# Performance work log

Hardware: AMD Instinct MI355X
Metric: run time of the kernel (lower is better)

Reference implementation:

```python
import jax, jax.numpy as jnp
import numpy as np

HEADS = 4
DIM_HEAD = 64
EPS = 1e-12  # F.normalize clamp_min eps

def _l2norm(t):
    n = jnp.sqrt(jnp.sum(t * t, axis=-1, keepdims=True))
    return t / jnp.maximum(n, EPS)

def _dwconv3d(x, w, groups):
    # x: [b, c, d, h, w]; w: [c, 1, 3, 3, 3]
    return jax.lax.conv_general_dilated(
        x, w, window_strides=(1, 1, 1),
        padding=((1, 1), (1, 1), (1, 1)),
        dimension_numbers=('NCDHW', 'OIDHW', 'NCDHW'),
        feature_group_count=groups)

def setup_inputs() -> dict:
    key = jax.random.key(0)
    ks = jax.random.split(key, 6)
    dim, inner = 64, HEADS * DIM_HEAD
    x_in = jax.random.normal(ks[0], (1, 8, 128, 128, dim), jnp.float32)
    w_qkv = jax.random.normal(ks[1], (dim, 3 * inner), jnp.float32) * 0.05
    rescale = jnp.ones((HEADS, 1, 1), jnp.float32)
    w_proj = jax.random.normal(ks[2], (inner, dim), jnp.float32) * 0.05
    b_proj = jax.random.normal(ks[3], (dim,), jnp.float32) * 0.01
    w_pe1 = jax.random.normal(ks[4], (dim, 1, 3, 3, 3), jnp.float32) * 0.1
    w_pe2 = jax.random.normal(ks[5], (dim, 1, 3, 3, 3), jnp.float32) * 0.1
    return {"x_in": x_in, "w_qkv": w_qkv, "rescale": rescale,
            "w_proj": w_proj, "b_proj": b_proj, "w_pe1": w_pe1, "w_pe2": w_pe2}

def reference(x_in, w_qkv, rescale, w_proj, b_proj, w_pe1, w_pe2):
    b, d, h, w, c = x_in.shape
    N = d * h * w
    inner = HEADS * DIM_HEAD
    x = x_in.reshape(b, N, c)
    qkv = x @ w_qkv  # [b, N, 3*inner]
    q, k, v = jnp.split(qkv, 3, axis=-1)
    # [b, N, inner] -> [b, heads, dim_head, N]
    to_hdn = lambda t: t.reshape(b, N, HEADS, DIM_HEAD).transpose(0, 2, 3, 1)
    q, k, v = to_hdn(q), to_hdn(k), to_hdn(v)
    q = _l2norm(q)
    k = _l2norm(k)
    attn = jnp.einsum('bhdn,bhen->bhde', k, q)  # [b, heads, dd, dd]
    attn = attn * rescale[None]
    attn = jax.nn.softmax(attn, axis=-1)
    xo = jnp.einsum('bhde,bhen->bhdn', attn, v)  # [b, heads, dd, N]
    xo = xo.transpose(0, 3, 1, 2).reshape(b, N, inner)  # (h dd) channel order
    out_c = (xo @ w_proj + b_proj).reshape(b, d, h, w, c)
    # positional branch: depthwise conv3d -> GELU -> depthwise conv3d
    xp = x_in.transpose(0, 4, 1, 2, 3)  # [b, c, d, h, w]
    xp = _dwconv3d(xp, w_pe1, c)
    xp = jax.nn.gelu(xp, approximate=False)
    xp = _dwconv3d(xp, w_pe2, c)
    out_p = xp.transpose(0, 2, 3, 4, 1)
    return out_c + out_p
```

## Files before the change

### kernel.cpp

```cpp
#include <hip/hip_runtime.h>
#include <hip/hip_bf16.h>
#include <math.h>


#define NTOK 131072

__device__ __forceinline__ uint32_t pk2(float a, float b) {
    return ((__float_as_uint(a) + 0x8000u) >> 16) |
           (((__float_as_uint(b) + 0x8000u) >> 16) << 16);
}
__device__ __forceinline__ float bl(uint32_t w) { return __uint_as_float(w << 16); }
__device__ __forceinline__ float bh(uint32_t w) { return __uint_as_float(w & 0xFFFF0000u); }

__global__ __launch_bounds__(256) void k_gram(const float* __restrict__ x,
                                              float* __restrict__ partial) {
    __shared__ float xs[16][64];
    const int tid = threadIdx.x;
    const int col = tid & 63;
    const int g = tid >> 6;
    float acc[16];
#pragma unroll
    for (int i = 0; i < 16; ++i) acc[i] = 0.f;
    const long tok0 = (long)blockIdx.x * 128;
    for (int t0 = 0; t0 < 128; t0 += 16) {
        __syncthreads();
        const float4* src = (const float4*)(x + (tok0 + t0) * 64);
        ((float4*)&xs[0][0])[tid] = src[tid];
        __syncthreads();
#pragma unroll
        for (int t = 0; t < 16; ++t) {
            const float xa = xs[t][col];
#pragma unroll
            for (int j = 0; j < 16; j += 4) {
                const float4 lv = *(const float4*)&xs[t][g * 16 + j];
                acc[j + 0] += lv.x * xa;
                acc[j + 1] += lv.y * xa;
                acc[j + 2] += lv.z * xa;
                acc[j + 3] += lv.w * xa;
            }
        }
    }
    float* p = partial + (size_t)blockIdx.x * 4096;
#pragma unroll
    for (int i = 0; i < 16; ++i) p[(g * 16 + i) * 64 + col] = acc[i];
}

__global__ __launch_bounds__(256) void k_reduceG(const float* __restrict__ partial,
                                                 float* __restrict__ G) {
    const int pslice = blockIdx.x >> 4;
    const int eblk = blockIdx.x & 15;
    const int e = eblk * 256 + threadIdx.x;
    const float* p = partial + (size_t)pslice * 64 * 4096 + e;
    float s = 0.f;
#pragma unroll 8
    for (int i = 0; i < 64; ++i) s += p[(size_t)i * 4096];
    atomicAdd(&G[e], s);
}

__global__ __launch_bounds__(512) void k_attn(const float* __restrict__ G,
                                              const float* __restrict__ w_qkv,
                                              const float* __restrict__ rescale,
                                              const float* __restrict__ w_proj,
                                              float* __restrict__ wf) {
    __shared__ float smem[6 * 4096 + 64 * 65];
    float (*Gs)[64] = (float(*)[64])smem;
    float (*PT)[64] = (float(*)[64])smem;
    float (*Bq)[64] = (float(*)[64])(smem + 4096);
    float (*Bk)[64] = (float(*)[64])(smem + 8192);
    float (*Bp)[64] = (float(*)[64])(smem + 12288);
    float (*M1)[64] = (float(*)[64])(smem + 16384);
    float (*M2)[64] = (float(*)[64])(smem + 20480);
    float (*Sb)[65] = (float(*)[65])(smem + 24576);
    __shared__ float qin[64], kin[64];

    const int h = blockIdx.x;
    const int tid = threadIdx.x;
    const int lane = tid & 63;
    const int g = tid >> 6;
    const int p0 = g * 8;

    for (int idx = tid; idx < 4096; idx += 512) {
        const int a = idx >> 6, e = idx & 63;
        Gs[a][e] = G[idx];
        Bq[a][e] = w_qkv[a * 768 + h * 64 + e];
        Bk[a][e] = w_qkv[a * 768 + 256 + h * 64 + e];
        Bp[a][e] = w_proj[(h * 64 + a) * 64 + e];
    }
    __syncthreads();

    {
        float acc[8];
#pragma unroll
        for (int i = 0; i < 8; ++i) acc[i] = 0.f;
        for (int a = 0; a < 64; ++a) {
            const float r = Bq[a][lane];
            const float4 l0 = *(const float4*)&Gs[a][p0];
            const float4 l1 = *(const float4*)&Gs[a][p0 + 4];
            acc[0] += l0.x * r; acc[1] += l0.y * r; acc[2] += l0.z * r; acc[3] += l0.w * r;
            acc[4] += l1.x * r; acc[5] += l1.y * r; acc[6] += l1.z * r; acc[7] += l1.w * r;
        }
#pragma unroll
        for (int i = 0; i < 8; ++i) M1[p0 + i][lane] = acc[i];
    }
    {
        float acc[8];
#pragma unroll
        for (int i = 0; i < 8; ++i) acc[i] = 0.f;
        for (int a = 0; a < 64; ++a) {
            const float r = Bk[a][lane];
            const float4 l0 = *(const float4*)&Gs[a][p0];
            const float4 l1 = *(const float4*)&Gs[a][p0 + 4];
            acc[0] += l0.x * r; acc[1] += l0.y * r; acc[2] += l0.z * r; acc[3] += l0.w * r;
            acc[4] += l1.x * r; acc[5] += l1.y * r; acc[6] += l1.z * r; acc[7] += l1.w * r;
        }
#pragma unroll
        for (int i = 0; i < 8; ++i) M2[p0 + i][lane] = acc[i];
    }
    __syncthreads();

    if (tid < 64) {
        float s = 0.f;
        for (int a = 0; a < 64; ++a) s += Bq[a][tid] * M1[a][tid];
        qin[tid] = 1.f / fmaxf(sqrtf(s), 1e-12f);
    } else if (tid < 128) {
        const int d = tid - 64;
        float s = 0.f;
        for (int a = 0; a < 64; ++a) s += Bk[a][d] * M2[a][d];
        kin[d] = 1.f / fmaxf(sqrtf(s), 1e-12f);
    }
    __syncthreads();

    const float rs = rescale[h];
    {
        float acc[8];
#pragma unroll
        for (int i = 0; i < 8; ++i) acc[i] = 0.f;
        for (int a = 0; a < 64; ++a) {
            const float r = M1[a][lane];
            const float4 l0 = *(const float4*)&Bk[a][p0];
            const float4 l1 = *(const float4*)&Bk[a][p0 + 4];
            acc[0] += l0.x * r; acc[1] += l0.y * r; acc[2] += l0.z * r; acc[3] += l0.w * r;
            acc[4] += l1.x * r; acc[5] += l1.y * r; acc[6] += l1.z * r; acc[7] += l1.w * r;
        }
        const float qv = qin[lane] * rs;
#pragma unroll
        for (int i = 0; i < 8; ++i) Sb[p0 + i][lane] = acc[i] * (kin[p0 + i] * qv);
    }
    for (int idx = tid; idx < 4096; idx += 512) {
        const int a = idx >> 6, e = idx & 63;
        Bq[e][a] = w_qkv[a * 768 + 512 + h * 64 + e];
    }
    __syncthreads();

    if (tid < 64) {
        const int d = tid;
        float m = -1e30f;
        for (int e = 0; e < 64; ++e) m = fmaxf(m, Sb[d][e]);
        float s = 0.f;
        for (int e = 0; e < 64; ++e) {
            const float pv = expf(Sb[d][e] - m);
            s += pv;
            PT[e][d] = pv;
        }
        const float inv = 1.f / s;
        for (int e = 0; e < 64; ++e) PT[e][d] *= inv;
    }
    __syncthreads();

    {
        float acc[8];
#pragma unroll
        for (int i = 0; i < 8; ++i) acc[i] = 0.f;
        for (int e = 0; e < 64; ++e) {
            const float r = Bq[e][lane];
            const float4 l0 = *(const float4*)&PT[e][p0];
            const float4 l1 = *(const float4*)&PT[e][p0 + 4];
            acc[0] += l0.x * r; acc[1] += l0.y * r; acc[2] += l0.z * r; acc[3] += l0.w * r;
            acc[4] += l1.x * r; acc[5] += l1.y * r; acc[6] += l1.z * r; acc[7] += l1.w * r;
        }
        __syncthreads();
#pragma unroll
        for (int i = 0; i < 8; ++i) M2[p0 + i][lane] = acc[i];
    }
    __syncthreads();

    {
        float acc[8];
#pragma unroll
        for (int i = 0; i < 8; ++i) acc[i] = 0.f;
        for (int d = 0; d < 64; ++d) {
            const float r = Bp[d][lane];
            const float4 l0 = *(const float4*)&M2[d][p0];
            const float4 l1 = *(const float4*)&M2[d][p0 + 4];
            acc[0] += l0.x * r; acc[1] += l0.y * r; acc[2] += l0.z * r; acc[3] += l0.w * r;
            acc[4] += l1.x * r; acc[5] += l1.y * r; acc[6] += l1.z * r; acc[7] += l1.w * r;
        }
#pragma unroll
        for (int i = 0; i < 8; ++i) atomicAdd(&wf[(p0 + i) * 64 + lane], acc[i]);
    }
}

__global__ __launch_bounds__(256) void k_out(const float* __restrict__ x,
                                             const float* __restrict__ wf_g,
                                             const float* __restrict__ b_proj,
                                             float* __restrict__ out) {
    __shared__ float wfs[64][64];
    __shared__ float xs[64][64];
    const int tid = threadIdx.x;
    const int c = tid & 63;
    const int q = tid >> 6;
    for (int idx = tid; idx < 4096; idx += 256) wfs[idx >> 6][idx & 63] = wf_g[idx];
    __syncthreads();
    float wf[64];
#pragma unroll
    for (int j = 0; j < 64; ++j) wf[j] = wfs[j][c];
    const float bb = b_proj[c];
    const long base = (long)blockIdx.x * 256;
    for (int s = 0; s < 4; ++s) {
        const long v0 = base + s * 64;
        __syncthreads();
        const float4* src = (const float4*)(x + v0 * 64);
#pragma unroll
        for (int r = 0; r < 4; ++r) ((float4*)&xs[0][0])[tid + r * 256] = src[tid + r * 256];
        __syncthreads();
#pragma unroll
        for (int vi = 0; vi < 16; ++vi) {
            const int v = q * 16 + vi;
            float acc = bb;
#pragma unroll
            for (int j = 0; j < 64; j += 4) {
                const float4 xr = *(const float4*)&xs[v][j];
                acc += xr.x * wf[j] + xr.y * wf[j + 1] + xr.z * wf[j + 2] + xr.w * wf[j + 3];
            }
            out[(v0 + v) * 64 + c] = acc;
        }
    }
}

__global__ __launch_bounds__(256) void k_conv(const float* __restrict__ x,
                                              const float* __restrict__ w1,
                                              const float* __restrict__ w2,
                                              float* __restrict__ out) {
    __shared__ uint32_t xt[12][12][8][6];
    __shared__ uint32_t y1[10][10][8][6];
    const int tid = threadIdx.x;
    const int b = blockIdx.x;
    const int xcd = b & 7, seq = (b >> 3) & 31, cg = b >> 8;
    const int tile = xcd * 32 + seq;
    const int tw = tile & 15, th = tile >> 4;
    const int h0 = th * 8, w0 = tw * 8;
    const int c = tid & 7;
    const int cglob = cg * 8 + c;

    float wr1[27];
#pragma unroll
    for (int o = 0; o < 27; ++o) wr1[o] = w1[cglob * 27 + o];

    for (int e = tid; e < 1152; e += 256) {
        const int sp = e >> 3;
        const int hh = sp / 12;
        const int ww = sp - hh * 12;
        const int gh = h0 + hh - 2, gw = w0 + ww - 2;
        uint32_t col[6] = {0u, 0u, 0u, 0u, 0u, 0u};
        if ((unsigned)gh < 128u && (unsigned)gw < 128u) {
            const float* xp = x + ((long)gh * 128 + gw) * 64 + cglob;
            float v[8];
#pragma unroll
            for (int gd = 0; gd < 8; ++gd) v[gd] = xp[(long)gd * 1048576];
            col[1] = pk2(v[0], v[1]);
            col[2] = pk2(v[2], v[3]);
            col[3] = pk2(v[4], v[5]);
            col[4] = pk2(v[6], v[7]);
        }
        uint32_t* dst = &xt[hh][ww][e & 7][0];
        *(uint2*)(dst + 0) = make_uint2(col[0], col[1]);
        *(uint2*)(dst + 2) = make_uint2(col[2], col[3]);
        *(uint2*)(dst + 4) = make_uint2(col[4], col[5]);
    }
    __syncthreads();

    for (int e = tid; e < 800; e += 256) {
        const int sp = e >> 3;
        const int hi_ = sp / 10;
        const int wi = sp - hi_ * 10;
        const int ghp = h0 + hi_ - 1, gwp = w0 + wi - 1;
        uint32_t ow_[6];
        if ((unsigned)ghp < 128u && (unsigned)gwp < 128u) {
            float acc[8];
#pragma unroll
            for (int j = 0; j < 8; ++j) acc[j] = 0.f;
#pragma unroll
            for (int oh = 0; oh < 3; ++oh) {
#pragma unroll
                for (int ow = 0; ow < 3; ++ow) {
                    const uint32_t* cp = &xt[hi_ + oh][wi + ow][e & 7][0];
                    const uint2 wa = *(const uint2*)(cp + 0);
                    const uint2 wb = *(const uint2*)(cp + 2);
                    const uint2 wc = *(const uint2*)(cp + 4);
                    float xc[12];
                    xc[1] = bh(wa.x);
                    xc[2] = bl(wa.y); xc[3] = bh(wa.y);
                    xc[4] = bl(wb.x); xc[5] = bh(wb.x);
                    xc[6] = bl(wb.y); xc[7] = bh(wb.y);
                    xc[8] = bl(wc.x); xc[9] = bh(wc.x);
                    xc[10] = bl(wc.y);
                    const float wg0 = wr1[oh * 3 + ow];
                    const float wg1 = wr1[9 + oh * 3 + ow];
                    const float wg2 = wr1[18 + oh * 3 + ow];
#pragma unroll
                    for (int j = 0; j < 8; ++j)
                        acc[j] += wg0 * xc[j + 1] + wg1 * xc[j + 2] + wg2 * xc[j + 3];
                }
            }
            float gl[8];
#pragma unroll
            for (int j = 0; j < 8; ++j)
                gl[j] = 0.5f * acc[j] * (1.f + erff(acc[j] * 0.70710678118654752f));
            ow_[0] = pk2(0.f, gl[0]);
            ow_[1] = pk2(gl[1], gl[2]);
            ow_[2] = pk2(gl[3], gl[4]);
            ow_[3] = pk2(gl[5], gl[6]);
            ow_[4] = pk2(gl[7], 0.f);
            ow_[5] = 0u;
        } else {
#pragma unroll
            for (int i = 0; i < 6; ++i) ow_[i] = 0u;
        }
        uint32_t* dst = &y1[hi_][wi][e & 7][0];
        *(uint2*)(dst + 0) = make_uint2(ow_[0], ow_[1]);
        *(uint2*)(dst + 2) = make_uint2(ow_[2], ow_[3]);
        *(uint2*)(dst + 4) = make_uint2(ow_[4], ow_[5]);
    }

    float wr2[27];
#pragma unroll
    for (int o = 0; o < 27; ++o) wr2[o] = w2[cglob * 27 + o];
    __syncthreads();

    for (int e = tid; e < 512; e += 256) {
        const int sp = e >> 3;
        const int ho = sp >> 3, wo = sp & 7;
        float a2[8];
#pragma unroll
        for (int j = 0; j < 8; ++j) a2[j] = 0.f;
#pragma unroll
        for (int oh = 0; oh < 3; ++oh) {
#pragma unroll
            for (int ow = 0; ow < 3; ++ow) {
                const uint32_t* cp = &y1[ho + oh][wo + ow][e & 7][0];
                const uint2 wa = *(const uint2*)(cp + 0);
                const uint2 wb = *(const uint2*)(cp + 2);
                const uint32_t wcw = cp[4];
                float yc[10];
                yc[0] = bl(wa.x); yc[1] = bh(wa.x);
                yc[2] = bl(wa.y); yc[3] = bh(wa.y);
                yc[4] = bl(wb.x); yc[5] = bh(wb.x);
                yc[6] = bl(wb.y); yc[7] = bh(wb.y);
                yc[8] = bl(wcw);  yc[9] = bh(wcw);
                const float wg0 = wr2[oh * 3 + ow];
                const float wg1 = wr2[9 + oh * 3 + ow];
                const float wg2 = wr2[18 + oh * 3 + ow];
#pragma unroll
                for (int j = 0; j < 8; ++j)
                    a2[j] += wg0 * yc[j] + wg1 * yc[j + 1] + wg2 * yc[j + 2];
            }
        }
        const int gh = h0 + ho, gw = w0 + wo;
        float* op = out + ((long)gh * 128 + gw) * 64 + cglob;
#pragma unroll
        for (int j = 0; j < 8; ++j) op[(long)j * 1048576] += a2[j];
    }
}

extern "C" void kernel_launch(void* const* d_in, const int* in_sizes, int n_in,
                              void* d_out, int out_size, void* d_ws, size_t ws_size,
                              hipStream_t stream) {
    const float* x       = (const float*)d_in[0];
    const float* w_qkv   = (const float*)d_in[1];
    const float* rescale = (const float*)d_in[2];
    const float* w_proj  = (const float*)d_in[3];
    const float* b_proj  = (const float*)d_in[4];
    const float* w_pe1   = (const float*)d_in[5];
    const float* w_pe2   = (const float*)d_in[6];
    float* out = (float*)d_out;

    float* G  = (float*)d_ws;
    float* wf = G + 4096;
    float* partial = out;

    hipMemsetAsync(G, 0, 8192 * sizeof(float), stream);
    k_gram<<<1024, 256, 0, stream>>>(x, partial);
    k_reduceG<<<256, 256, 0, stream>>>(partial, G);
    k_attn<<<4, 512, 0, stream>>>(G, w_qkv, rescale, w_proj, wf);
    k_out<<<512, 256, 0, stream>>>(x, wf, b_proj, out);
    k_conv<<<2048, 256, 0, stream>>>(x, w_pe1, w_pe2, out);
}
```

Measured before the change: 234.8 us.

## Compute Gram matrix with split-bf16 MFMA and shrink conv LDS layout

The Gram-matrix kernel now uses bf16 MFMA instructions with a hi/lo split of fp32 inputs (three products) to keep near-fp32 accuracy. Only the upper-triangular 16x16 tiles are computed, and the reduce kernel maps symmetric entries back onto them. This replaces the scalar FMA loop with matrix-core work and shrinks the partial buffer. Separately, the conv kernel's LDS column stride drops from 6 to 5 words, which cuts shared-memory footprint and may change bank conflicts, though loads go from uint2 to scalar.

```diff
diff --git a/kernel.cpp b/kernel.cpp
--- a/kernel.cpp
+++ b/kernel.cpp
@@ -5,6 +5,9 @@
 
 #define NTOK 131072
 
+typedef __attribute__((ext_vector_type(8))) short short8v;
+typedef __attribute__((ext_vector_type(4))) float f32x4;
+
 __device__ __forceinline__ uint32_t pk2(float a, float b) {
     return ((__float_as_uint(a) + 0x8000u) >> 16) |
            (((__float_as_uint(b) + 0x8000u) >> 16) << 16);
@@ -14,47 +17,69 @@
 
 __global__ __launch_bounds__(256) void k_gram(const float* __restrict__ x,
                                               float* __restrict__ partial) {
-    __shared__ float xs[16][64];
     const int tid = threadIdx.x;
-    const int col = tid & 63;
-    const int g = tid >> 6;
-    float acc[16];
-#pragma unroll
-    for (int i = 0; i < 16; ++i) acc[i] = 0.f;
-    const long tok0 = (long)blockIdx.x * 128;
-    for (int t0 = 0; t0 < 128; t0 += 16) {
-        __syncthreads();
-        const float4* src = (const float4*)(x + (tok0 + t0) * 64);
-        ((float4*)&xs[0][0])[tid] = src[tid];
-        __syncthreads();
-#pragma unroll
-        for (int t = 0; t < 16; ++t) {
-            const float xa = xs[t][col];
-#pragma unroll
-            for (int j = 0; j < 16; j += 4) {
-                const float4 lv = *(const float4*)&xs[t][g * 16 + j];
-                acc[j + 0] += lv.x * xa;
-                acc[j + 1] += lv.y * xa;
-                acc[j + 2] += lv.z * xa;
-                acc[j + 3] += lv.w * xa;
+    const int lane = tid & 63;
+    const int wave = tid >> 6;
+    const int gwave = blockIdx.x * 4 + wave;
+    const int lh = lane >> 4;
+    const int lc = lane & 15;
+    f32x4 acc[10];
+#pragma unroll
+    for (int t = 0; t < 10; ++t) acc[t] = (f32x4){0.f, 0.f, 0.f, 0.f};
+    const long tokBase = (long)gwave * 64;
+#pragma unroll
+    for (int s = 0; s < 2; ++s) {
+        const long t0 = tokBase + s * 32 + lh * 8;
+        float v[4][8];
+#pragma unroll
+        for (int r = 0; r < 4; ++r) {
+            const float* p = x + t0 * 64 + r * 16 + lc;
+#pragma unroll
+            for (int i = 0; i < 8; ++i) v[r][i] = p[i * 64];
+        }
+        union { short8v s8; uint32_t u[4]; } fh[4], fl[4];
+#pragma unroll
+        for (int r = 0; r < 4; ++r) {
+#pragma unroll
+            for (int w = 0; w < 4; ++w) {
+                const float a = v[r][2 * w], b = v[r][2 * w + 1];
+                const uint32_t hw = pk2(a, b);
+                fh[r].u[w] = hw;
+                fl[r].u[w] = pk2(a - bl(hw), b - bh(hw));
             }
         }
-    }
-    float* p = partial + (size_t)blockIdx.x * 4096;
-#pragma unroll
-    for (int i = 0; i < 16; ++i) p[(g * 16 + i) * 64 + col] = acc[i];
+#pragma unroll
+        for (int td = 0; td < 4; ++td) {
+#pragma unroll
+            for (int te = td; te < 4; ++te) {
+                const int t = td * 4 + te - (td * (td + 1)) / 2;
+                acc[t] = __builtin_amdgcn_mfma_f32_16x16x32_bf16(fh[td].s8, fh[te].s8, acc[t], 0, 0, 0);
+                acc[t] = __builtin_amdgcn_mfma_f32_16x16x32_bf16(fh[td].s8, fl[te].s8, acc[t], 0, 0, 0);
+                acc[t] = __builtin_amdgcn_mfma_f32_16x16x32_bf16(fl[td].s8, fh[te].s8, acc[t], 0, 0, 0);
+            }
+        }
+    }
+    float* pb = partial + (size_t)gwave * 2560;
+#pragma unroll
+    for (int t = 0; t < 10; ++t)
+#pragma unroll
+        for (int j = 0; j < 4; ++j)
+            pb[t * 256 + (lh * 4 + j) * 16 + lc] = acc[t][j];
 }
 
 __global__ __launch_bounds__(256) void k_reduceG(const float* __restrict__ partial,
                                                  float* __restrict__ G) {
-    const int pslice = blockIdx.x >> 4;
-    const int eblk = blockIdx.x & 15;
-    const int e = eblk * 256 + threadIdx.x;
-    const float* p = partial + (size_t)pslice * 64 * 4096 + e;
+    const int entry = (blockIdx.x & 15) * 256 + threadIdx.x;
+    const int slice = blockIdx.x >> 4;
+    const int d = entry >> 6, e = entry & 63;
+    int td = d >> 4, te = e >> 4, r = d & 15, c = e & 15;
+    if (td > te) { int t = td; td = te; te = t; t = r; r = c; c = t; }
+    const int off = (td * 4 + te - (td * (td + 1)) / 2) * 256 + r * 16 + c;
+    const float* p = partial + (size_t)slice * 64 * 2560 + off;
     float s = 0.f;
 #pragma unroll 8
-    for (int i = 0; i < 64; ++i) s += p[(size_t)i * 4096];
-    atomicAdd(&G[e], s);
+    for (int i = 0; i < 64; ++i) s += p[(size_t)i * 2560];
+    atomicAdd(&G[entry], s);
 }
 
 __global__ __launch_bounds__(512) void k_attn(const float* __restrict__ G,
@@ -241,8 +266,8 @@
                                               const float* __restrict__ w1,
                                               const float* __restrict__ w2,
                                               float* __restrict__ out) {
-    __shared__ uint32_t xt[12][12][8][6];
-    __shared__ uint32_t y1[10][10][8][6];
+    __shared__ uint32_t xt[12][12][8][5];
+    __shared__ uint32_t y1[10][10][8][5];
     const int tid = threadIdx.x;
     const int b = blockIdx.x;
     const int xcd = b & 7, seq = (b >> 3) & 31, cg = b >> 8;
@@ -261,21 +286,21 @@
         const int hh = sp / 12;
         const int ww = sp - hh * 12;
         const int gh = h0 + hh - 2, gw = w0 + ww - 2;
-        uint32_t col[6] = {0u, 0u, 0u, 0u, 0u, 0u};
+        uint32_t col[5] = {0u, 0u, 0u, 0u, 0u};
         if ((unsigned)gh < 128u && (unsigned)gw < 128u) {
             const float* xp = x + ((long)gh * 128 + gw) * 64 + cglob;
             float v[8];
 #pragma unroll
             for (int gd = 0; gd < 8; ++gd) v[gd] = xp[(long)gd * 1048576];
-            col[1] = pk2(v[0], v[1]);
-            col[2] = pk2(v[2], v[3]);
-            col[3] = pk2(v[4], v[5]);
-            col[4] = pk2(v[6], v[7]);
+            col[0] = pk2(0.f, v[0]);
+            col[1] = pk2(v[1], v[2]);
+            col[2] = pk2(v[3], v[4]);
+            col[3] = pk2(v[5], v[6]);
+            col[4] = pk2(v[7], 0.f);
         }
         uint32_t* dst = &xt[hh][ww][e & 7][0];
-        *(uint2*)(dst + 0) = make_uint2(col[0], col[1]);
-        *(uint2*)(dst + 2) = make_uint2(col[2], col[3]);
-        *(uint2*)(dst + 4) = make_uint2(col[4], col[5]);
+#pragma unroll
+        for (int i = 0; i < 5; ++i) dst[i] = col[i];
     }
     __syncthreads();
 
@@ -284,7 +309,7 @@
         const int hi_ = sp / 10;
         const int wi = sp - hi_ * 10;
         const int ghp = h0 + hi_ - 1, gwp = w0 + wi - 1;
-        uint32_t ow_[6];
+        uint32_t ow_[5];
         if ((unsigned)ghp < 128u && (unsigned)gwp < 128u) {
             float acc[8];
 #pragma unroll
@@ -294,16 +319,13 @@
 #pragma unroll
                 for (int ow = 0; ow < 3; ++ow) {
                     const uint32_t* cp = &xt[hi_ + oh][wi + ow][e & 7][0];
-                    const uint2 wa = *(const uint2*)(cp + 0);
-                    const uint2 wb = *(const uint2*)(cp + 2);
-                    const uint2 wc = *(const uint2*)(cp + 4);
-                    float xc[12];
-                    xc[1] = bh(wa.x);
-                    xc[2] = bl(wa.y); xc[3] = bh(wa.y);
-                    xc[4] = bl(wb.x); xc[5] = bh(wb.x);
-                    xc[6] = bl(wb.y); xc[7] = bh(wb.y);
-                    xc[8] = bl(wc.x); xc[9] = bh(wc.x);
-                    xc[10] = bl(wc.y);
+                    float xc[11];
+#pragma unroll
+                    for (int wdx = 0; wdx < 5; ++wdx) {
+                        const uint32_t wv = cp[wdx];
+                        xc[2 * wdx + 1] = bl(wv);
+                        xc[2 * wdx + 2] = bh(wv);
+                    }
                     const float wg0 = wr1[oh * 3 + ow];
                     const float wg1 = wr1[9 + oh * 3 + ow];
                     const float wg2 = wr1[18 + oh * 3 + ow];
@@ -321,15 +343,13 @@
             ow_[2] = pk2(gl[3], gl[4]);
             ow_[3] = pk2(gl[5], gl[6]);
             ow_[4] = pk2(gl[7], 0.f);
-            ow_[5] = 0u;
         } else {
 #pragma unroll
-            for (int i = 0; i < 6; ++i) ow_[i] = 0u;
+            for (int i = 0; i < 5; ++i) ow_[i] = 0u;
         }
         uint32_t* dst = &y1[hi_][wi][e & 7][0];
-        *(uint2*)(dst + 0) = make_uint2(ow_[0], ow_[1]);
-        *(uint2*)(dst + 2) = make_uint2(ow_[2], ow_[3]);
-        *(uint2*)(dst + 4) = make_uint2(ow_[4], ow_[5]);
+#pragma unroll
+        for (int i = 0; i < 5; ++i) dst[i] = ow_[i];
     }
 
     float wr2[27];
@@ -348,15 +368,13 @@
 #pragma unroll
             for (int ow = 0; ow < 3; ++ow) {
                 const uint32_t* cp = &y1[ho + oh][wo + ow][e & 7][0];
-                const uint2 wa = *(const uint2*)(cp + 0);
-                const uint2 wb = *(const uint2*)(cp + 2);
-                const uint32_t wcw = cp[4];
                 float yc[10];
-                yc[0] = bl(wa.x); yc[1] = bh(wa.x);
-                yc[2] = bl(wa.y); yc[3] = bh(wa.y);
-                yc[4] = bl(wb.x); yc[5] = bh(wb.x);
-                yc[6] = bl(wb.y); yc[7] = bh(wb.y);
-                yc[8] = bl(wcw);  yc[9] = bh(wcw);
+#pragma unroll
+                for (int wdx = 0; wdx < 5; ++wdx) {
+                    const uint32_t wv = cp[wdx];
+                    yc[2 * wdx] = bl(wv);
+                    yc[2 * wdx + 1] = bh(wv);
+                }
                 const float wg0 = wr2[oh * 3 + ow];
                 const float wg1 = wr2[9 + oh * 3 + ow];
                 const float wg2 = wr2[18 + oh * 3 + ow];
@@ -389,8 +407,8 @@
     float* partial = out;
 
     hipMemsetAsync(G, 0, 8192 * sizeof(float), stream);
-    k_gram<<<1024, 256, 0, stream>>>(x, partial);
-    k_reduceG<<<256, 256, 0, stream>>>(partial, G);
+    k_gram<<<512, 256, 0, stream>>>(x, partial);
+    k_reduceG<<<512, 256, 0, stream>>>(partial, G);
     k_attn<<<4, 512, 0, stream>>>(G, w_qkv, rescale, w_proj, wf);
     k_out<<<512, 256, 0, stream>>>(x, wf, b_proj, out);
     k_conv<<<2048, 256, 0, stream>>>(x, w_pe1, w_pe2, out);
```

New measurement: 233.3 us. No clear change (-0.6%).
